# Kernel optimization log

Measured on AMD Instinct MI355X. Metric: run time of the kernel, lower is better.

Reference implementation:

```python
import jax, jax.numpy as jnp
import numpy as np

B, N, IN_DIM = 2, 2048, 1024
HEADS, HEAD_DIM = 16, 64

def setup_inputs() -> dict:
    key = jax.random.key(0)
    k1, k2, k3, k4, k5 = jax.random.split(key, 5)
    s_in = 1.0 / np.sqrt(IN_DIM)
    s_h = 1.0 / np.sqrt(HEADS * HEAD_DIM)
    return {
        "x": jax.random.normal(k1, (B, N, IN_DIM), jnp.float32),
        "w_qkv": jax.random.normal(k2, (IN_DIM, 3 * HEADS * HEAD_DIM), jnp.float32) * s_in,
        "b_qkv": jax.random.normal(k3, (3 * HEADS * HEAD_DIM,), jnp.float32) * s_in,
        "w_proj": jax.random.normal(k4, (HEADS * HEAD_DIM, IN_DIM), jnp.float32) * s_h,
        "b_proj": jax.random.normal(k5, (IN_DIM,), jnp.float32) * s_h,
    }

def reference(x, w_qkv, b_qkv, w_proj, b_proj):
    b, n, _ = x.shape
    scale = HEAD_DIM ** (-0.5)
    qkv = x @ w_qkv + b_qkv                               # (B,N,3*H*D)
    # torch: reshape(B,N,H,3*D).permute(0,2,1,3) then chunk last dim into q,k,v
    qkv = qkv.reshape(b, n, HEADS, 3 * HEAD_DIM).transpose(0, 2, 1, 3)  # (B,H,N,3D)
    q, k, v = jnp.split(qkv, 3, axis=-1)                  # each (B,H,N,D)
    attn = jnp.einsum("bhqd,bhkd->bhqk", q, k) * scale    # (B,H,N,N)
    attn = jax.nn.softmax(attn, axis=-1)
    out = jnp.einsum("bhqk,bhkd->bhqd", attn, v)          # (B,H,N,D)
    out = out.transpose(0, 2, 1, 3).reshape(b, n, HEADS * HEAD_DIM)
    return out @ w_proj + b_proj
```

## Files before the change

### kernel.cpp

```cpp
#include <hip/hip_runtime.h>
#include <hip/hip_bf16.h>
#include <cstdint>
#include <cstddef>

#define BD 2
#define SEQ 2048
#define NH 16
#define HD 64
#define IND 1024
#define QKVD 3072
#define MROWS (BD * SEQ)

typedef __attribute__((ext_vector_type(8))) short s8v;
typedef __attribute__((ext_vector_type(4))) short s4v;
typedef __attribute__((ext_vector_type(4))) float f4v;

__device__ __forceinline__ short f2bf(float f) {
  __hip_bfloat16 h = __float2bfloat16(f);
  return *reinterpret_cast<short*>(&h);
}

__device__ __forceinline__ void async_copy16(void* lds, const void* g) {
  __builtin_amdgcn_global_load_lds(
      (const __attribute__((address_space(1))) unsigned int*)g,
      (__attribute__((address_space(3))) unsigned int*)lds, 16, 0, 0);
}

__device__ __forceinline__ const s8v* lds_frag(const short* p, int row, int col) {
  int byte = (row << 7) + (col << 1);
  byte ^= ((row & 7) << 4);
  return (const s8v*)((const char*)p + byte);
}

__global__ void k_cast(const float* __restrict__ in, short* __restrict__ out, int n4) {
  int i = blockIdx.x * blockDim.x + threadIdx.x;
  if (i >= n4) return;
  float4 v = reinterpret_cast<const float4*>(in)[i];
  s4v o;
  o[0] = f2bf(v.x); o[1] = f2bf(v.y); o[2] = f2bf(v.z); o[3] = f2bf(v.w);
  reinterpret_cast<s4v*>(out)[i] = o;
}

__global__ void k_transpose_cast(const float* __restrict__ w, short* __restrict__ wT,
                                 int R, int C) {
  __shared__ float tile[32][33];
  int c0 = blockIdx.x * 32, r0 = blockIdx.y * 32;
  int tx = threadIdx.x, ty = threadIdx.y;
  #pragma unroll
  for (int j = 0; j < 32; j += 8)
    tile[ty + j][tx] = w[(size_t)(r0 + ty + j) * C + c0 + tx];
  __syncthreads();
  #pragma unroll
  for (int j = 0; j < 32; j += 8)
    wT[(size_t)(c0 + ty + j) * R + r0 + tx] = f2bf(tile[tx][ty + j]);
}

template <int MODE>
__global__ __launch_bounds__(256) void k_gemm(const short* __restrict__ A,
                                              const short* __restrict__ BT,
                                              const float* __restrict__ bias,
                                              short* __restrict__ obf,
                                              float* __restrict__ ofl,
                                              int Mr, int Nc, int K) {
  constexpr int BM = 128, BN = 128, BK = 32;
  __shared__ short As[BM][BK];
  __shared__ short Bs[BN][BK];
  const int rm = blockIdx.x * BM, cn = blockIdx.y * BN;
  const int t = threadIdx.x, l = t & 63;
  const int wm = (t >> 6) >> 1, wn = (t >> 6) & 1;
  const int lr = l & 15, lc = l >> 4;

  f4v acc[4][4];
  #pragma unroll
  for (int m = 0; m < 4; ++m)
    #pragma unroll
    for (int n = 0; n < 4; ++n) acc[m][n] = (f4v)0.0f;

  for (int k0 = 0; k0 < K; k0 += BK) {
    __syncthreads();
    #pragma unroll
    for (int p = 0; p < 2; ++p) {
      int c = p * 256 + t;
      async_copy16(&As[c >> 2][(c & 3) * 8],
                   &A[(size_t)(rm + (c >> 2)) * K + k0 + (c & 3) * 8]);
      async_copy16(&Bs[c >> 2][(c & 3) * 8],
                   &BT[(size_t)(cn + (c >> 2)) * K + k0 + (c & 3) * 8]);
    }
    __syncthreads();
    s8v af[4], bf[4];
    #pragma unroll
    for (int m = 0; m < 4; ++m)
      af[m] = *(const s8v*)&As[wm * 64 + m * 16 + lr][lc * 8];
    #pragma unroll
    for (int n = 0; n < 4; ++n)
      bf[n] = *(const s8v*)&Bs[wn * 64 + n * 16 + lr][lc * 8];
    #pragma unroll
    for (int m = 0; m < 4; ++m)
      #pragma unroll
      for (int n = 0; n < 4; ++n)
        acc[m][n] = __builtin_amdgcn_mfma_f32_16x16x32_bf16(af[m], bf[n], acc[m][n], 0, 0, 0);
  }

  const int row0 = rm + wm * 64, col0 = cn + wn * 64;
  #pragma unroll
  for (int n = 0; n < 4; ++n) {
    const int col = col0 + n * 16 + lr;
    const float bv = bias[col];
    if (MODE == 0) {
      const int h = col / 192, rem = col % 192;
      const int wch = rem >> 6, d = rem & 63;
      const float scale = (wch == 0) ? 0.125f : 1.0f;
      short* dst = obf + (size_t)wch * ((size_t)BD * NH * SEQ * HD);
      #pragma unroll
      for (int m = 0; m < 4; ++m)
        #pragma unroll
        for (int r = 0; r < 4; ++r) {
          const int row = row0 + m * 16 + lc * 4 + r;
          const int b = row >> 11, nn = row & (SEQ - 1);
          const short val = f2bf((acc[m][n][r] + bv) * scale);
          if (wch == 2)
            dst[((size_t)(b * NH + h) * HD + d) * SEQ + nn] = val;
          else
            dst[((size_t)(b * NH + h) * SEQ + nn) * HD + d] = val;
        }
    } else {
      #pragma unroll
      for (int m = 0; m < 4; ++m)
        #pragma unroll
        for (int r = 0; r < 4; ++r) {
          const int row = row0 + m * 16 + lc * 4 + r;
          ofl[(size_t)row * Nc + col] = acc[m][n][r] + bv;
        }
    }
  }
}

__global__ __launch_bounds__(256) void k_attn(const short* __restrict__ Qw,
                                              const short* __restrict__ Kw,
                                              const short* __restrict__ Vt_g,
                                              short* __restrict__ AO) {
  const int qb = blockIdx.x, bh = blockIdx.y;
  const size_t base = (size_t)bh * SEQ * HD;
  const int t = threadIdx.x, l = t & 63, w = t >> 6;
  const int lr = l & 15, lc = l >> 4;
  __shared__ short Ks[64 * 64];
  __shared__ short Vt[64 * 64];
  __shared__ short Ps[4][16 * 64];
  const int q0 = qb * 64 + w * 16;

  s8v qf[2];
  #pragma unroll
  for (int s = 0; s < 2; ++s)
    qf[s] = *(const s8v*)&Qw[base + (size_t)(q0 + lr) * HD + s * 32 + lc * 8];

  f4v of[4];
  #pragma unroll
  for (int j = 0; j < 4; ++j) of[j] = (f4v)0.0f;
  float Mx = -3.0e38f, Ls = 0.0f;
  short* Pw = &Ps[w][0];

  for (int kv = 0; kv < SEQ; kv += 64) {
    __syncthreads();
    #pragma unroll
    for (int p = 0; p < 2; ++p) {
      int c = p * 256 + t;
      int row = c >> 3, ch = (c & 7) ^ (row & 7);
      async_copy16((char*)Ks + c * 16,
                   &Kw[base + (size_t)(kv + row) * HD + ch * 8]);
    }
    #pragma unroll
    for (int p = 0; p < 2; ++p) {
      int c = p * 256 + t;
      int row = c >> 3, ch = (c & 7) ^ (row & 7);
      async_copy16((char*)Vt + c * 16,
                   &Vt_g[base + (size_t)row * SEQ + kv + ch * 8]);
    }
    __syncthreads();

    f4v st[4];
    #pragma unroll
    for (int j = 0; j < 4; ++j) st[j] = (f4v)0.0f;
    #pragma unroll
    for (int j = 0; j < 4; ++j)
      #pragma unroll
      for (int s = 0; s < 2; ++s) {
        s8v kf = *lds_frag(Ks, j * 16 + lr, s * 32 + lc * 8);
        st[j] = __builtin_amdgcn_mfma_f32_16x16x32_bf16(kf, qf[s], st[j], 0, 0, 0);
      }

    float pm = -3.0e38f;
    #pragma unroll
    for (int j = 0; j < 4; ++j)
      #pragma unroll
      for (int r = 0; r < 4; ++r) pm = fmaxf(pm, st[j][r]);
    pm = fmaxf(pm, __shfl_xor(pm, 16));
    pm = fmaxf(pm, __shfl_xor(pm, 32));
    const float Mn = fmaxf(Mx, pm);
    const float alpha = __expf(Mx - Mn);
    float rs = 0.0f;
    #pragma unroll
    for (int j = 0; j < 4; ++j) {
      s4v pk;
      #pragma unroll
      for (int r = 0; r < 4; ++r) {
        const float p = __expf(st[j][r] - Mn);
        rs += p;
        pk[r] = f2bf(p);
      }
      int byte = (lr << 7) + ((j * 16 + lc * 4) << 1);
      byte ^= ((lr & 7) << 4);
      *(s4v*)((char*)Pw + byte) = pk;
    }
    rs += __shfl_xor(rs, 16);
    rs += __shfl_xor(rs, 32);
    Ls = Ls * alpha + rs;
    Mx = Mn;

    float al[4];
    #pragma unroll
    for (int r = 0; r < 4; ++r) al[r] = __shfl(alpha, lc * 4 + r);
    #pragma unroll
    for (int jd = 0; jd < 4; ++jd)
      #pragma unroll
      for (int r = 0; r < 4; ++r) of[jd][r] *= al[r];

    #pragma unroll
    for (int s = 0; s < 2; ++s) {
      s8v pf = *lds_frag(Pw, lr, s * 32 + lc * 8);
      #pragma unroll
      for (int jd = 0; jd < 4; ++jd) {
        s8v vf = *lds_frag(Vt, jd * 16 + lr, s * 32 + lc * 8);
        of[jd] = __builtin_amdgcn_mfma_f32_16x16x32_bf16(pf, vf, of[jd], 0, 0, 0);
      }
    }
  }

  float li[4];
  #pragma unroll
  for (int r = 0; r < 4; ++r) li[r] = 1.0f / __shfl(Ls, lc * 4 + r);
  const int b = bh >> 4, h = bh & 15;
  #pragma unroll
  for (int jd = 0; jd < 4; ++jd)
    #pragma unroll
    for (int r = 0; r < 4; ++r) {
      const int nq = q0 + lc * 4 + r;
      AO[(size_t)(b * SEQ + nq) * (NH * HD) + h * HD + jd * 16 + lr] =
          f2bf(of[jd][r] * li[r]);
    }
}

extern "C" void kernel_launch(void* const* d_in, const int* in_sizes, int n_in,
                              void* d_out, int out_size, void* d_ws, size_t ws_size,
                              hipStream_t stream) {
  const float* x      = (const float*)d_in[0];
  const float* w_qkv  = (const float*)d_in[1];
  const float* b_qkv  = (const float*)d_in[2];
  const float* w_proj = (const float*)d_in[3];
  const float* b_proj = (const float*)d_in[4];
  float* out = (float*)d_out;

  char* ws = (char*)d_ws;
  short* xb  = (short*)(ws);
  short* wqT = (short*)(ws + 8388608);
  short* wpT = (short*)(ws + 14680064);
  short* Qw  = (short*)(ws + 16777216);
  short* Kw  = (short*)(ws + 25165824);
  short* Vtg = (short*)(ws + 33554432);
  short* AO  = (short*)(ws + 41943040);

  k_cast<<<(MROWS * IND / 4 + 255) / 256, 256, 0, stream>>>(x, xb, MROWS * IND / 4);
  dim3 tb(32, 8);
  k_transpose_cast<<<dim3(QKVD / 32, IND / 32), tb, 0, stream>>>(w_qkv, wqT, IND, QKVD);
  k_transpose_cast<<<dim3(IND / 32, IND / 32), tb, 0, stream>>>(w_proj, wpT, IND, IND);

  k_gemm<0><<<dim3(MROWS / 128, QKVD / 128), 256, 0, stream>>>(
      xb, wqT, b_qkv, Qw, nullptr, MROWS, QKVD, IND);
  k_attn<<<dim3(SEQ / 64, BD * NH), 256, 0, stream>>>(Qw, Kw, Vtg, AO);
  k_gemm<1><<<dim3(MROWS / 128, IND / 128), 256, 0, stream>>>(
      AO, wpT, b_proj, nullptr, out, MROWS, IND, IND);
}
```

Baseline: 154.9 us.

## Double-buffer K/V tiles in attention kernel to overlap loads with compute

The attention kernel now keeps two LDS buffers each for K and V^T. It issues the async global-to-LDS copy of the next KV tile before computing on the current tile, so load latency can hide behind the MFMA and softmax work. Per-thread copy offsets are precomputed outside the loop, which cuts one of the two barriers per iteration. This doubles LDS use for K/V, which may reduce occupancy. It also adds an explicit lgkmcnt wait before the P·V stage.

```diff
diff --git a/kernel.cpp b/kernel.cpp
--- a/kernel.cpp
+++ b/kernel.cpp
@@ -10,6 +10,7 @@
 #define IND 1024
 #define QKVD 3072
 #define MROWS (BD * SEQ)
+#define NT (SEQ / 64)
 
 typedef __attribute__((ext_vector_type(8))) short s8v;
 typedef __attribute__((ext_vector_type(4))) short s4v;
@@ -143,10 +144,22 @@
   const size_t base = (size_t)bh * SEQ * HD;
   const int t = threadIdx.x, l = t & 63, w = t >> 6;
   const int lr = l & 15, lc = l >> 4;
-  __shared__ short Ks[64 * 64];
-  __shared__ short Vt[64 * 64];
+  __shared__ short Ks[2][64 * 64];
+  __shared__ short Vt[2][64 * 64];
   __shared__ short Ps[4][16 * 64];
   const int q0 = qb * 64 + w * 16;
+
+  int ldsOff[2], kOff[2], vOff[2];
+  #pragma unroll
+  for (int p = 0; p < 2; ++p) {
+    const int c = p * 256 + t;
+    const int row = c >> 3, ch = (c & 7) ^ (row & 7);
+    ldsOff[p] = c * 16;
+    kOff[p] = row * HD + ch * 8;
+    vOff[p] = row * SEQ + ch * 8;
+  }
+  const short* Kb = Kw + base;
+  const short* Vb = Vt_g + base;
 
   s8v qf[2];
   #pragma unroll
@@ -159,24 +172,17 @@
   float Mx = -3.0e38f, Ls = 0.0f;
   short* Pw = &Ps[w][0];
 
-  for (int kv = 0; kv < SEQ; kv += 64) {
-    __syncthreads();
-    #pragma unroll
-    for (int p = 0; p < 2; ++p) {
-      int c = p * 256 + t;
-      int row = c >> 3, ch = (c & 7) ^ (row & 7);
-      async_copy16((char*)Ks + c * 16,
-                   &Kw[base + (size_t)(kv + row) * HD + ch * 8]);
-    }
-    #pragma unroll
-    for (int p = 0; p < 2; ++p) {
-      int c = p * 256 + t;
-      int row = c >> 3, ch = (c & 7) ^ (row & 7);
-      async_copy16((char*)Vt + c * 16,
-                   &Vt_g[base + (size_t)row * SEQ + kv + ch * 8]);
-    }
-    __syncthreads();
-
+  auto STAGE = [&](int buf, int tile) {
+    const size_t kv = (size_t)tile * 64;
+    #pragma unroll
+    for (int p = 0; p < 2; ++p)
+      async_copy16((char*)Ks[buf] + ldsOff[p], Kb + kv * HD + kOff[p]);
+    #pragma unroll
+    for (int p = 0; p < 2; ++p)
+      async_copy16((char*)Vt[buf] + ldsOff[p], Vb + kv + vOff[p]);
+  };
+
+  auto COMPUTE = [&](const short* ksB, const short* vtB) {
     f4v st[4];
     #pragma unroll
     for (int j = 0; j < 4; ++j) st[j] = (f4v)0.0f;
@@ -184,7 +190,7 @@
     for (int j = 0; j < 4; ++j)
       #pragma unroll
       for (int s = 0; s < 2; ++s) {
-        s8v kf = *lds_frag(Ks, j * 16 + lr, s * 32 + lc * 8);
+        s8v kf = *lds_frag(ksB, j * 16 + lr, s * 32 + lc * 8);
         st[j] = __builtin_amdgcn_mfma_f32_16x16x32_bf16(kf, qf[s], st[j], 0, 0, 0);
       }
 
@@ -224,16 +230,29 @@
       #pragma unroll
       for (int r = 0; r < 4; ++r) of[jd][r] *= al[r];
 
+    asm volatile("s_waitcnt lgkmcnt(0)" ::: "memory");
+
     #pragma unroll
     for (int s = 0; s < 2; ++s) {
       s8v pf = *lds_frag(Pw, lr, s * 32 + lc * 8);
       #pragma unroll
       for (int jd = 0; jd < 4; ++jd) {
-        s8v vf = *lds_frag(Vt, jd * 16 + lr, s * 32 + lc * 8);
+        s8v vf = *lds_frag(vtB, jd * 16 + lr, s * 32 + lc * 8);
         of[jd] = __builtin_amdgcn_mfma_f32_16x16x32_bf16(pf, vf, of[jd], 0, 0, 0);
       }
     }
+  };
+
+  STAGE(0, 0);
+  __syncthreads();
+  int cur = 0;
+  for (int tt = 0; tt < NT - 1; ++tt) {
+    STAGE(cur ^ 1, tt + 1);
+    COMPUTE(Ks[cur], Vt[cur]);
+    __syncthreads();
+    cur ^= 1;
   }
+  COMPUTE(Ks[cur], Vt[cur]);
 
   float li[4];
   #pragma unroll
```

After: 155.9 us. About the same (+0.6%).

## Split attention over KV into two halves and combine partials in a separate kernel

Applied to the files above, without the earlier changes.

Splits the attention KV loop into two halves across a new grid dimension, writing unnormalized fp32 partial outputs plus per-row max and sum. A new combine kernel merges the halves with log-sum-exp weights and writes the bf16 attention output. The goal is to double the number of blocks so more work is in flight, with a launch_bounds occupancy hint, hoisted address math, and an explicit LDS wait. The cost is extra fp32 partial traffic, reuse of the output buffer and workspace as scratch, and one more kernel launch.

```diff
diff --git a/kernel.cpp b/kernel.cpp
--- a/kernel.cpp
+++ b/kernel.cpp
@@ -10,6 +10,8 @@
 #define IND 1024
 #define QKVD 3072
 #define MROWS (BD * SEQ)
+#define NSPLIT 2
+#define TILES_PER_SPLIT (SEQ / 64 / NSPLIT)
 
 typedef __attribute__((ext_vector_type(8))) short s8v;
 typedef __attribute__((ext_vector_type(4))) short s4v;
@@ -135,11 +137,13 @@
   }
 }
 
-__global__ __launch_bounds__(256) void k_attn(const short* __restrict__ Qw,
-                                              const short* __restrict__ Kw,
-                                              const short* __restrict__ Vt_g,
-                                              short* __restrict__ AO) {
-  const int qb = blockIdx.x, bh = blockIdx.y;
+__global__ __launch_bounds__(256, 6) void k_attn(const short* __restrict__ Qw,
+                                                 const short* __restrict__ Kw,
+                                                 const short* __restrict__ Vt_g,
+                                                 float* __restrict__ OP0,
+                                                 float* __restrict__ OP1,
+                                                 float* __restrict__ ML) {
+  const int qb = blockIdx.x, bh = blockIdx.y, split = blockIdx.z;
   const size_t base = (size_t)bh * SEQ * HD;
   const int t = threadIdx.x, l = t & 63, w = t >> 6;
   const int lr = l & 15, lc = l >> 4;
@@ -148,6 +152,18 @@
   __shared__ short Ps[4][16 * 64];
   const int q0 = qb * 64 + w * 16;
 
+  int ldsOff[2], kOff[2], vOff[2];
+  #pragma unroll
+  for (int p = 0; p < 2; ++p) {
+    const int c = p * 256 + t;
+    const int row = c >> 3, ch = (c & 7) ^ (row & 7);
+    ldsOff[p] = c * 16;
+    kOff[p] = row * HD + ch * 8;
+    vOff[p] = row * SEQ + ch * 8;
+  }
+  const short* Kb = Kw + base;
+  const short* Vb = Vt_g + base;
+
   s8v qf[2];
   #pragma unroll
   for (int s = 0; s < 2; ++s)
@@ -159,22 +175,15 @@
   float Mx = -3.0e38f, Ls = 0.0f;
   short* Pw = &Ps[w][0];
 
-  for (int kv = 0; kv < SEQ; kv += 64) {
+  for (int tt = 0; tt < TILES_PER_SPLIT; ++tt) {
+    const size_t kv = (size_t)(split * TILES_PER_SPLIT + tt) * 64;
     __syncthreads();
     #pragma unroll
-    for (int p = 0; p < 2; ++p) {
-      int c = p * 256 + t;
-      int row = c >> 3, ch = (c & 7) ^ (row & 7);
-      async_copy16((char*)Ks + c * 16,
-                   &Kw[base + (size_t)(kv + row) * HD + ch * 8]);
-    }
-    #pragma unroll
-    for (int p = 0; p < 2; ++p) {
-      int c = p * 256 + t;
-      int row = c >> 3, ch = (c & 7) ^ (row & 7);
-      async_copy16((char*)Vt + c * 16,
-                   &Vt_g[base + (size_t)row * SEQ + kv + ch * 8]);
-    }
+    for (int p = 0; p < 2; ++p)
+      async_copy16((char*)Ks + ldsOff[p], Kb + kv * HD + kOff[p]);
+    #pragma unroll
+    for (int p = 0; p < 2; ++p)
+      async_copy16((char*)Vt + ldsOff[p], Vb + kv + vOff[p]);
     __syncthreads();
 
     f4v st[4];
@@ -224,6 +233,8 @@
       #pragma unroll
       for (int r = 0; r < 4; ++r) of[jd][r] *= al[r];
 
+    asm volatile("s_waitcnt lgkmcnt(0)" ::: "memory");
+
     #pragma unroll
     for (int s = 0; s < 2; ++s) {
       s8v pf = *lds_frag(Pw, lr, s * 32 + lc * 8);
@@ -235,18 +246,46 @@
     }
   }
 
-  float li[4];
-  #pragma unroll
-  for (int r = 0; r < 4; ++r) li[r] = 1.0f / __shfl(Ls, lc * 4 + r);
+  float* OP = split ? OP1 : OP0;
+  #pragma unroll
+  for (int jd = 0; jd < 4; ++jd)
+    #pragma unroll
+    for (int r = 0; r < 4; ++r)
+      OP[((size_t)bh * SEQ + q0 + lc * 4 + r) * HD + jd * 16 + lr] = of[jd][r];
+  if (lc == 0) {
+    float2 ml = make_float2(Mx, Ls);
+    *reinterpret_cast<float2*>(
+        &ML[((size_t)split * BD * NH * SEQ + (size_t)bh * SEQ + q0 + lr) * 2]) = ml;
+  }
+}
+
+__global__ __launch_bounds__(256) void k_comb(const float* __restrict__ OP0,
+                                              const float* __restrict__ OP1,
+                                              const float* __restrict__ ML,
+                                              short* __restrict__ AO) {
+  const int gid = blockIdx.x * 256 + threadIdx.x;
+  const int row = gid >> 2, c = gid & 3;
+  const int bh = row >> 11, q = row & (SEQ - 1);
+  const float2 ml1 = *reinterpret_cast<const float2*>(&ML[(size_t)row * 2]);
+  const float2 ml2 = *reinterpret_cast<const float2*>(
+      &ML[((size_t)BD * NH * SEQ + row) * 2]);
+  const float M = fmaxf(ml1.x, ml2.x);
+  const float w1 = __expf(ml1.x - M), w2 = __expf(ml2.x - M);
+  const float inv = 1.0f / (w1 * ml1.y + w2 * ml2.y);
   const int b = bh >> 4, h = bh & 15;
-  #pragma unroll
-  for (int jd = 0; jd < 4; ++jd)
-    #pragma unroll
-    for (int r = 0; r < 4; ++r) {
-      const int nq = q0 + lc * 4 + r;
-      AO[(size_t)(b * SEQ + nq) * (NH * HD) + h * HD + jd * 16 + lr] =
-          f2bf(of[jd][r] * li[r]);
-    }
+  short* dst = &AO[((size_t)(b * SEQ + q) * (NH * HD)) + h * HD + c * 16];
+  const size_t src = (size_t)row * HD + c * 16;
+  #pragma unroll
+  for (int i = 0; i < 4; ++i) {
+    float4 a = reinterpret_cast<const float4*>(&OP0[src])[i];
+    float4 bvv = reinterpret_cast<const float4*>(&OP1[src])[i];
+    s4v o;
+    o[0] = f2bf((w1 * a.x + w2 * bvv.x) * inv);
+    o[1] = f2bf((w1 * a.y + w2 * bvv.y) * inv);
+    o[2] = f2bf((w1 * a.z + w2 * bvv.z) * inv);
+    o[3] = f2bf((w1 * a.w + w2 * bvv.w) * inv);
+    reinterpret_cast<s4v*>(dst)[i] = o;
+  }
 }
 
 extern "C" void kernel_launch(void* const* d_in, const int* in_sizes, int n_in,
@@ -260,13 +299,16 @@
   float* out = (float*)d_out;
 
   char* ws = (char*)d_ws;
-  short* xb  = (short*)(ws);
-  short* wqT = (short*)(ws + 8388608);
-  short* wpT = (short*)(ws + 14680064);
-  short* Qw  = (short*)(ws + 16777216);
-  short* Kw  = (short*)(ws + 25165824);
-  short* Vtg = (short*)(ws + 33554432);
-  short* AO  = (short*)(ws + 41943040);
+  short* wpT = (short*)(ws);
+  short* Qw  = (short*)(ws + (2u << 20));
+  short* Kw  = (short*)(ws + (10u << 20));
+  short* Vtg = (short*)(ws + (18u << 20));
+  short* AO  = (short*)(ws + (26u << 20));
+  short* xb  = (short*)(ws + (34u << 20));
+  short* wqT = (short*)(ws + (42u << 20));
+  float* OP1 = (float*)(ws + (34u << 20));
+  float* ML  = (float*)(ws + (50u << 20));
+  float* OP0 = (float*)d_out;
 
   k_cast<<<(MROWS * IND / 4 + 255) / 256, 256, 0, stream>>>(x, xb, MROWS * IND / 4);
   dim3 tb(32, 8);
@@ -275,7 +317,8 @@
 
   k_gemm<0><<<dim3(MROWS / 128, QKVD / 128), 256, 0, stream>>>(
       xb, wqT, b_qkv, Qw, nullptr, MROWS, QKVD, IND);
-  k_attn<<<dim3(SEQ / 64, BD * NH), 256, 0, stream>>>(Qw, Kw, Vtg, AO);
+  k_attn<<<dim3(SEQ / 64, BD * NH, NSPLIT), 256, 0, stream>>>(Qw, Kw, Vtg, OP0, OP1, ML);
+  k_comb<<<(BD * NH * SEQ * 4) / 256, 256, 0, stream>>>(OP0, OP1, ML, AO);
   k_gemm<1><<<dim3(MROWS / 128, IND / 128), 256, 0, stream>>>(
       AO, wpT, b_proj, nullptr, out, MROWS, IND, IND);
 }
```

Measured after the change: 156.6 us. About the same (+1.1%).
